# Optimization experiments

Hardware: AMD Instinct MI355X
Metric: run time of the kernel (lower is better)

The kernel has to match this reference:

```python
import jax, jax.numpy as jnp
import numpy as np

B, C, D = 16384, 2048, 128
POS_PROB = 0.002  # ~33 positives per class on average
EPS_POOL = 1e-9
EPS_NORM = 1e-12


def _l2_normalize(x, axis=-1):
    return x * jax.lax.rsqrt(jnp.sum(x * x, axis=axis, keepdims=True) + EPS_NORM)


def setup_inputs() -> dict:
    key = jax.random.key(0)
    k1, k2, k3 = jax.random.split(key, 3)
    output = jax.random.normal(k1, (B, D), dtype=jnp.float32)
    class_emb = jax.random.normal(k2, (C, D), dtype=jnp.float32)
    targets = (jax.random.uniform(k3, (B, C)) < POS_PROB).astype(jnp.float32)
    temperature = jnp.float32(0.07)
    return {"output": output, "class_emb": class_emb, "targets": targets,
            "temperature": temperature}


def reference(output, class_emb, targets, temperature):
    dt = output.dtype
    # masked mean pooling per class: equivalent to tile->mask->sum/count_nonzero
    # counts[c,d] = #{b : targets[b,c]*output[b,d] != 0}
    t_nz = (targets != 0).astype(dt)            # [B,C]
    o_nz = (output != 0).astype(dt)             # [B,D]
    counts = jnp.einsum('bc,bd->cd', t_nz, o_nz)          # [C,D]
    pooled = jnp.einsum('bc,bd->cd', targets, output) / (counts + EPS_POOL)  # [C,D]
    # cosine similarities (avoid materializing [C,C,D] tiles)
    pn = _l2_normalize(pooled)                  # [C,D]
    en = _l2_normalize(class_emb)               # [C,D]
    all_cosine = pn @ en.T                      # [C,C]
    class_sim = en @ en.T                       # [C,C]
    # topk(-sim, C) then argsort == rank of each class by ascending similarity
    order = jnp.argsort(class_sim, axis=-1)     # ascending sim (== topk of -sim)
    rank = jnp.argsort(order, axis=-1)          # inverse permutation
    discount = jnp.log(rank.astype(dt) + 2.0)   # [C,C]
    logits = all_cosine / (temperature * discount)
    log_p = jax.nn.log_softmax(logits, axis=1)  # [C,C]
    pos_log_p = jnp.diagonal(log_p)             # [C] diagonal gather
    mask_count = jnp.sum(targets, axis=0)       # [C]
    valid = mask_count > 0
    n_valid = jnp.maximum(jnp.sum(valid.astype(dt)), 1.0)
    infonce_mean = jnp.sum(jnp.where(valid, -pos_log_p, 0.0)) / n_valid
    return infonce_mean
```

## Files before the change

### kernel.cpp

```cpp
#include <hip/hip_runtime.h>
#include <hip/hip_bf16.h>
#include <math.h>

#define B_SZ 16384
#define C_SZ 2048
#define D_SZ 128
#define MAXP 256
#define SCAN_BLOCKS 4096

typedef float f32x4 __attribute__((ext_vector_type(4)));
typedef short short8 __attribute__((ext_vector_type(8)));


__global__ __launch_bounds__(256) void k_pre(unsigned* __restrict__ zr) {
    int t = blockIdx.x * blockDim.x + threadIdx.x;
    if (t < 2112) zr[t] = 0u;
}

__global__ __launch_bounds__(256) void k_scan(const float* __restrict__ targets,
                                              const float* __restrict__ class_emb,
                                              int* __restrict__ pos_count,
                                              int* __restrict__ pos_list,
                                              __hip_bfloat16* __restrict__ enh,
                                              __hip_bfloat16* __restrict__ enl) {
    const int bid = blockIdx.x;
    if (bid >= SCAN_BLOCKS) {
        const int g = threadIdx.x >> 7;
        const int d = threadIdx.x & 127;
        const int c = ((bid - SCAN_BLOCKS) << 1) + g;
        __shared__ float s_w[2][2];
        float v = class_emb[c * D_SZ + d];
        float sq = v * v;
#pragma unroll
        for (int off = 32; off >= 1; off >>= 1) sq += __shfl_xor(sq, off);
        if ((d & 63) == 0) s_w[g][d >> 6] = sq;
        __syncthreads();
        float tot = s_w[g][0] + s_w[g][1];
        float vn = v * rsqrtf(tot + 1e-12f);
        __hip_bfloat16 h = __float2bfloat16(vn);
        enh[c * D_SZ + d] = h;
        enl[c * D_SZ + d] = __float2bfloat16(vn - __bfloat162float(h));
        return;
    }
    int tid = bid * 256 + threadIdx.x;
    int total = (B_SZ * C_SZ) >> 2;
    const int stride = SCAN_BLOCKS * 256;
    for (int v = tid; v < total; v += stride) {
        float4 t = ((const float4*)targets)[v];
        if (t.x != 0.f || t.y != 0.f || t.z != 0.f || t.w != 0.f) {
            int e0 = v << 2;
            int b = e0 >> 11;
            int c0 = e0 & (C_SZ - 1);
            float vals[4] = {t.x, t.y, t.z, t.w};
#pragma unroll
            for (int q = 0; q < 4; ++q) {
                if (vals[q] != 0.f) {
                    int c = c0 + q;
                    int slot = atomicAdd(&pos_count[c], 1);
                    if (slot < MAXP) pos_list[c * MAXP + slot] = b;
                }
            }
        }
    }
}

__global__ __launch_bounds__(256) void k_pool(const float* __restrict__ output,
                                              const int* __restrict__ pos_count,
                                              const int* __restrict__ pos_list,
                                              __hip_bfloat16* __restrict__ pnh,
                                              __hip_bfloat16* __restrict__ pnl) {
    int c = blockIdx.x;
    int d = threadIdx.x & 127;
    int half = threadIdx.x >> 7;
    __shared__ float s_acc[2][128];
    __shared__ float s_cnt[2][128];
    __shared__ float s_w[2];
    int n = pos_count[c];
    if (n > MAXP) n = MAXP;
    float acc = 0.f, cnt = 0.f;
    for (int k = half; k < n; k += 2) {
        int b = pos_list[c * MAXP + k];
        float v = output[b * D_SZ + d];
        acc += v;
        cnt += (v != 0.f) ? 1.f : 0.f;
    }
    s_acc[half][d] = acc;
    s_cnt[half][d] = cnt;
    __syncthreads();
    if (half == 0) {
        acc = s_acc[0][d] + s_acc[1][d];
        cnt = s_cnt[0][d] + s_cnt[1][d];
        float pooled = acc / (cnt + 1e-9f);
        float sq = pooled * pooled;
#pragma unroll
        for (int off = 32; off >= 1; off >>= 1) sq += __shfl_xor(sq, off);
        if ((d & 63) == 0) s_w[d >> 6] = sq;
        __syncthreads();
        float tot = s_w[0] + s_w[1];
        float vn = pooled * rsqrtf(tot + 1e-12f);
        __hip_bfloat16 h = __float2bfloat16(vn);
        pnh[c * D_SZ + d] = h;
        pnl[c * D_SZ + d] = __float2bfloat16(vn - __bfloat162float(h));
    } else {
        __syncthreads();
    }
}

__global__ __launch_bounds__(256) void k_gemm_mfma(const __hip_bfloat16* __restrict__ enh_p,
                                                   const __hip_bfloat16* __restrict__ enl_p,
                                                   const __hip_bfloat16* __restrict__ pnh_p,
                                                   const __hip_bfloat16* __restrict__ pnl_p,
                                                   float* __restrict__ sim,
                                                   float* __restrict__ cosm) {
    extern __shared__ char smem[];
    char* As = smem;
    char* Bs = smem + 32768;
    const int tid = threadIdx.x;
    const __hip_bfloat16* Ah;
    const __hip_bfloat16* Al;
    float* Out;
    int rb;
    if (blockIdx.y < 32) { Ah = enh_p; Al = enl_p; Out = sim;  rb = blockIdx.y << 6; }
    else                 { Ah = pnh_p; Al = pnl_p; Out = cosm; rb = (blockIdx.y - 32) << 6; }
    const int cb = blockIdx.x << 6;
    {
        int r = tid >> 2;
        int c0 = (tid & 3) << 5;
        int sw = (r & 7) << 4;
#pragma unroll
        for (int j = 0; j < 4; ++j) {
            int c = c0 + (j << 3);
            uint4 vh = *(const uint4*)&Ah[(rb + r) * D_SZ + c];
            *(uint4*)(As + r * 512 + ((2 * c) ^ sw)) = vh;
            uint4 vl = *(const uint4*)&Al[(rb + r) * D_SZ + c];
            *(uint4*)(As + r * 512 + ((512 + 2 * c) ^ sw) - 256) = vl;
            uint4 wh = *(const uint4*)&enh_p[(cb + r) * D_SZ + c];
            *(uint4*)(Bs + r * 512 + ((2 * c) ^ sw)) = wh;
            uint4 wl = *(const uint4*)&enl_p[(cb + r) * D_SZ + c];
            *(uint4*)(Bs + r * 512 + ((512 + 2 * c) ^ sw) - 256) = wl;
        }
    }
    __syncthreads();
    const int w = tid >> 6, lane = tid & 63;
    const int wr = (w >> 1) << 5;
    const int wc = (w & 1) << 5;
    const int lrow = lane & 15;
    const int lk = (lane >> 4) << 4;
    int ar0 = wr + lrow, ar1 = wr + 16 + lrow;
    int br0 = wc + lrow, br1 = wc + 16 + lrow;
    const char* pa0 = As + ar0 * 512; const int swa0 = (ar0 & 7) << 4;
    const char* pa1 = As + ar1 * 512; const int swa1 = (ar1 & 7) << 4;
    const char* pb0 = Bs + br0 * 512; const int swb0 = (br0 & 7) << 4;
    const char* pb1 = Bs + br1 * 512; const int swb1 = (br1 & 7) << 4;
    f32x4 acc00 = {0.f, 0.f, 0.f, 0.f};
    f32x4 acc01 = acc00, acc10 = acc00, acc11 = acc00;
#pragma unroll
    for (int term = 0; term < 3; ++term) {
        const int ao = (term == 2) ? 256 : 0;
        const int bo = (term == 1) ? 256 : 0;
#pragma unroll
        for (int kk = 0; kk < 4; ++kk) {
            const int ka = ao + (kk << 6) + lk;
            const int kb = bo + (kk << 6) + lk;
            short8 a0 = *(const short8*)(pa0 + ((ka & 0x100) | ((ka & 0xFF) ^ swa0)));
            short8 a1 = *(const short8*)(pa1 + ((ka & 0x100) | ((ka & 0xFF) ^ swa1)));
            short8 b0 = *(const short8*)(pb0 + ((kb & 0x100) | ((kb & 0xFF) ^ swb0)));
            short8 b1 = *(const short8*)(pb1 + ((kb & 0x100) | ((kb & 0xFF) ^ swb1)));
            acc00 = __builtin_amdgcn_mfma_f32_16x16x32_bf16(a0, b0, acc00, 0, 0, 0);
            acc01 = __builtin_amdgcn_mfma_f32_16x16x32_bf16(a0, b1, acc01, 0, 0, 0);
            acc10 = __builtin_amdgcn_mfma_f32_16x16x32_bf16(a1, b0, acc10, 0, 0, 0);
            acc11 = __builtin_amdgcn_mfma_f32_16x16x32_bf16(a1, b1, acc11, 0, 0, 0);
        }
    }
    const int crow = rb + wr + ((lane >> 4) << 2);
    const int ccol = cb + wc + lrow;
#pragma unroll
    for (int r = 0; r < 4; ++r) {
        Out[(crow + r) * C_SZ + ccol]           = acc00[r];
        Out[(crow + r) * C_SZ + ccol + 16]      = acc01[r];
        Out[(crow + 16 + r) * C_SZ + ccol]      = acc10[r];
        Out[(crow + 16 + r) * C_SZ + ccol + 16] = acc11[r];
    }
}

__global__ __launch_bounds__(512) void k_rank_softmax(const float* __restrict__ sim,
                                                      const float* __restrict__ cosm,
                                                      const int* __restrict__ pos_count,
                                                      const float* __restrict__ tempPtr,
                                                      float* __restrict__ acc) {
    const int i0 = blockIdx.x << 1;
    __shared__ unsigned s_keys[2][C_SZ];
    __shared__ unsigned short s_idx[2][C_SZ];
    __shared__ unsigned s_hist[2][C_SZ / 2];
    __shared__ int s_wt[2][8];
    __shared__ float s_reds[2][8];
    __shared__ float s_diag[2];
    const int tid = threadIdx.x;
    const int lane = tid & 63;
    const int w = tid >> 6;
    const int base = tid << 2;
    const float M = 21.0f;
    const float temp = tempPtr[0];

    const bool v0 = pos_count[i0] != 0;
    const bool v1 = pos_count[i0 + 1] != 0;

    float4 sa0 = *(const float4*)&sim[i0 * C_SZ + base];
    float4 sa1 = *(const float4*)&sim[(i0 + 1) * C_SZ + base];
    float4 ca0 = *(const float4*)&cosm[i0 * C_SZ + base];
    float4 ca1 = *(const float4*)&cosm[(i0 + 1) * C_SZ + base];
    {
        uint4 z4 = {0u, 0u, 0u, 0u};
        ((uint4*)s_hist)[tid] = z4;
    }
    float xs0[4] = {sa0.x, sa0.y, sa0.z, sa0.w};
    float xs1[4] = {sa1.x, sa1.y, sa1.z, sa1.w};
    unsigned uk0[4], uk1[4];
    int bk0[4], bk1[4];
#pragma unroll
    for (int e = 0; e < 4; ++e) {
        unsigned u = __float_as_uint(xs0[e]);
        u = (u & 0x80000000u) ? ~u : (u | 0x80000000u);
        if (u == 0x7FFFFFFFu) u = 0x80000000u;
        uk0[e] = u;
        int b = (int)((xs0[e] + 0.5f) * 2047.0f);
        bk0[e] = b < 0 ? 0 : (b > 2047 ? 2047 : b);
        unsigned u1 = __float_as_uint(xs1[e]);
        u1 = (u1 & 0x80000000u) ? ~u1 : (u1 | 0x80000000u);
        if (u1 == 0x7FFFFFFFu) u1 = 0x80000000u;
        uk1[e] = u1;
        int b1 = (int)((xs1[e] + 0.5f) * 2047.0f);
        bk1[e] = b1 < 0 ? 0 : (b1 > 2047 ? 2047 : b1);
    }
    __syncthreads();
    if (v0) {
#pragma unroll
        for (int e = 0; e < 4; ++e)
            atomicAdd(&s_hist[0][bk0[e] >> 1], 1u << ((bk0[e] & 1) << 4));
    }
    if (v1) {
#pragma unroll
        for (int e = 0; e < 4; ++e)
            atomicAdd(&s_hist[1][bk1[e] >> 1], 1u << ((bk1[e] & 1) << 4));
    }
    __syncthreads();
    unsigned w00 = s_hist[0][2 * tid], w01 = s_hist[0][2 * tid + 1];
    unsigned w10 = s_hist[1][2 * tid], w11 = s_hist[1][2 * tid + 1];
    unsigned c00 = w00 & 0xFFFF, c01 = w00 >> 16, c02 = w01 & 0xFFFF, c03 = w01 >> 16;
    unsigned c10 = w10 & 0xFFFF, c11 = w10 >> 16, c12 = w11 & 0xFFFF, c13 = w11 >> 16;
    unsigned sum0 = c00 + c01 + c02 + c03;
    unsigned sum1 = c10 + c11 + c12 + c13;
    int incl0 = (int)sum0, incl1 = (int)sum1;
#pragma unroll
    for (int off = 1; off < 64; off <<= 1) {
        int o0 = __shfl_up(incl0, off);
        int o1 = __shfl_up(incl1, off);
        if (lane >= off) { incl0 += o0; incl1 += o1; }
    }
    if (lane == 63) { s_wt[0][w] = incl0; s_wt[1][w] = incl1; }
    __syncthreads();
    int wb0 = 0, wb1 = 0;
#pragma unroll
    for (int ww = 0; ww < 8; ++ww) {
        wb0 += (ww < w) ? s_wt[0][ww] : 0;
        wb1 += (ww < w) ? s_wt[1][ww] : 0;
    }
    unsigned eb0 = (unsigned)(wb0 + incl0 - (int)sum0);
    unsigned eb1 = (unsigned)(wb1 + incl1 - (int)sum1);
    {
        unsigned e00 = eb0, e01 = eb0 + c00, e02 = eb0 + c00 + c01, e03 = eb0 + c00 + c01 + c02;
        s_hist[0][2 * tid]     = e00 | (e01 << 16);
        s_hist[0][2 * tid + 1] = e02 | (e03 << 16);
        unsigned e10 = eb1, e11 = eb1 + c10, e12 = eb1 + c10 + c11, e13 = eb1 + c10 + c11 + c12;
        s_hist[1][2 * tid]     = e10 | (e11 << 16);
        s_hist[1][2 * tid + 1] = e12 | (e13 << 16);
    }
    __syncthreads();
    if (v0) {
#pragma unroll
        for (int e = 0; e < 4; ++e) {
            int sh = (bk0[e] & 1) << 4;
            unsigned old = atomicAdd(&s_hist[0][bk0[e] >> 1], 1u << sh);
            unsigned pos = (old >> sh) & 0xFFFFu;
            s_keys[0][pos] = uk0[e];
            s_idx[0][pos] = (unsigned short)(base + e);
        }
    }
    if (v1) {
#pragma unroll
        for (int e = 0; e < 4; ++e) {
            int sh = (bk1[e] & 1) << 4;
            unsigned old = atomicAdd(&s_hist[1][bk1[e] >> 1], 1u << sh);
            unsigned pos = (old >> sh) & 0xFFFFu;
            s_keys[1][pos] = uk1[e];
            s_idx[1][pos] = (unsigned short)(base + e);
        }
    }
    __syncthreads();
    float ls0 = 0.f, ls1 = 0.f;
    float cs0[4] = {ca0.x, ca0.y, ca0.z, ca0.w};
    float cs1[4] = {ca1.x, ca1.y, ca1.z, ca1.w};
    if (v0) {
        float lg0[4];
#pragma unroll
        for (int e = 0; e < 4; ++e) {
            int b = bk0[e];
            unsigned endv = (s_hist[0][b >> 1] >> ((b & 1) << 4)) & 0xFFFFu;
            unsigned startv = b ? ((s_hist[0][(b - 1) >> 1] >> (((b - 1) & 1) << 4)) & 0xFFFFu) : 0u;
            unsigned mk = uk0[e];
            int less = 0, eq = 0;
            for (unsigned j = startv; j < endv; ++j) {
                unsigned kj = s_keys[0][j];
                less += (kj < mk) ? 1 : 0;
                eq += (kj == mk) ? 1 : 0;
            }
            if (eq > 1) {
                unsigned myi = (unsigned)(base + e);
                for (unsigned j = startv; j < endv; ++j)
                    if (s_keys[0][j] == mk && (unsigned)s_idx[0][j] < myi) less++;
            }
            int rk = (int)startv + less;
            float den = temp * __logf((float)rk + 2.0f);
            lg0[e] = __fdividef(cs0[e], den);
            ls0 += __expf(lg0[e] - M);
        }
        if ((i0 >> 2) == tid) {
            int ei = i0 & 3;
            float dv = lg0[0];
#pragma unroll
            for (int e = 1; e < 4; ++e) dv = (ei == e) ? lg0[e] : dv;
            s_diag[0] = dv;
        }
    }
    if (v1) {
        float lg1[4];
#pragma unroll
        for (int e = 0; e < 4; ++e) {
            int b = bk1[e];
            unsigned endv = (s_hist[1][b >> 1] >> ((b & 1) << 4)) & 0xFFFFu;
            unsigned startv = b ? ((s_hist[1][(b - 1) >> 1] >> (((b - 1) & 1) << 4)) & 0xFFFFu) : 0u;
            unsigned mk = uk1[e];
            int less = 0, eq = 0;
            for (unsigned j = startv; j < endv; ++j) {
                unsigned kj = s_keys[1][j];
                less += (kj < mk) ? 1 : 0;
                eq += (kj == mk) ? 1 : 0;
            }
            if (eq > 1) {
                unsigned myi = (unsigned)(base + e);
                for (unsigned j = startv; j < endv; ++j)
                    if (s_keys[1][j] == mk && (unsigned)s_idx[1][j] < myi) less++;
            }
            int rk = (int)startv + less;
            float den = temp * __logf((float)rk + 2.0f);
            lg1[e] = __fdividef(cs1[e], den);
            ls1 += __expf(lg1[e] - M);
        }
        if (((i0 + 1) >> 2) == tid) {
            int ei = (i0 + 1) & 3;
            float dv = lg1[0];
#pragma unroll
            for (int e = 1; e < 4; ++e) dv = (ei == e) ? lg1[e] : dv;
            s_diag[1] = dv;
        }
    }
#pragma unroll
    for (int off = 1; off < 64; off <<= 1) {
        ls0 += __shfl_xor(ls0, off);
        ls1 += __shfl_xor(ls1, off);
    }
    if (lane == 0) { s_reds[0][w] = ls0; s_reds[1][w] = ls1; }
    __syncthreads();
    if (tid == 0) {
        float t0 = 0.f, t1 = 0.f;
#pragma unroll
        for (int ww = 0; ww < 8; ++ww) { t0 += s_reds[0][ww]; t1 += s_reds[1][ww]; }
        float lp = 0.f, nv = 0.f;
        if (v0) { lp += -(s_diag[0] - M - logf(t0)); nv += 1.f; }
        if (v1) { lp += -(s_diag[1] - M - logf(t1)); nv += 1.f; }
        if (nv > 0.f) {
            atomicAdd(&acc[0], lp);
            atomicAdd(&acc[1], nv);
        }
    }
}

__global__ void k_final(const float* __restrict__ acc, float* __restrict__ out) {
    out[0] = acc[0] / fmaxf(acc[1], 1.0f);
}

extern "C" void kernel_launch(void* const* d_in, const int* in_sizes, int n_in,
                              void* d_out, int out_size, void* d_ws, size_t ws_size,
                              hipStream_t stream) {
    const float* output    = (const float*)d_in[0];
    const float* class_emb = (const float*)d_in[1];
    const float* targets   = (const float*)d_in[2];
    const float* tempPtr   = (const float*)d_in[3];
    float* out = (float*)d_out;
    char* ws = (char*)d_ws;

    int*   pos_count = (int*)(ws + 0);
    float* acc       = (float*)(ws + 8192);
    int*   pos_list  = (int*)(ws + 8448);
    __hip_bfloat16* pnh = (__hip_bfloat16*)(ws + 2105600);
    __hip_bfloat16* pnl = (__hip_bfloat16*)(ws + 2629888);
    __hip_bfloat16* enh = (__hip_bfloat16*)(ws + 3154176);
    __hip_bfloat16* enl = (__hip_bfloat16*)(ws + 3678464);
    float* sim       = (float*)(ws + 4210944);
    float* cosm      = (float*)(ws + 20988160);

    k_pre<<<9, 256, 0, stream>>>((unsigned*)ws);
    k_scan<<<SCAN_BLOCKS + C_SZ / 2, 256, 0, stream>>>(targets, class_emb,
                                                       pos_count, pos_list, enh, enl);
    k_pool<<<C_SZ, 256, 0, stream>>>(output, pos_count, pos_list, pnh, pnl);
    dim3 g(C_SZ / 64, 2 * C_SZ / 64);
    k_gemm_mfma<<<g, 256, 65536, stream>>>(enh, enl, pnh, pnl, sim, cosm);
    k_rank_softmax<<<C_SZ / 2, 512, 0, stream>>>(sim, cosm, pos_count, tempPtr, acc);
    k_final<<<1, 1, 0, stream>>>(acc, out);
}
```

Baseline: 105.0 us.

## Rewrite rank-softmax as one-wavefront-per-row kernel with per-row partials and block reduction

```diff
diff --git a/kernel.cpp b/kernel.cpp
--- a/kernel.cpp
+++ b/kernel.cpp
@@ -14,7 +14,7 @@
 
 __global__ __launch_bounds__(256) void k_pre(unsigned* __restrict__ zr) {
     int t = blockIdx.x * blockDim.x + threadIdx.x;
-    if (t < 2112) zr[t] = 0u;
+    if (t < C_SZ) zr[t] = 0u;
 }
 
 __global__ __launch_bounds__(256) void k_scan(const float* __restrict__ targets,
@@ -183,210 +183,158 @@
     }
 }
 
-__global__ __launch_bounds__(512) void k_rank_softmax(const float* __restrict__ sim,
-                                                      const float* __restrict__ cosm,
-                                                      const int* __restrict__ pos_count,
-                                                      const float* __restrict__ tempPtr,
-                                                      float* __restrict__ acc) {
-    const int i0 = blockIdx.x << 1;
-    __shared__ unsigned s_keys[2][C_SZ];
-    __shared__ unsigned short s_idx[2][C_SZ];
-    __shared__ unsigned s_hist[2][C_SZ / 2];
-    __shared__ int s_wt[2][8];
-    __shared__ float s_reds[2][8];
-    __shared__ float s_diag[2];
-    const int tid = threadIdx.x;
-    const int lane = tid & 63;
-    const int w = tid >> 6;
-    const int base = tid << 2;
+__device__ __forceinline__ int bucket_of(unsigned u) {
+    float x = (u & 0x80000000u) ? __uint_as_float(u & 0x7FFFFFFFu)
+                                : __uint_as_float(~u);
+    int b = (int)((x + 0.5f) * 2047.0f);
+    return b < 0 ? 0 : (b > 2047 ? 2047 : b);
+}
+
+__global__ __launch_bounds__(64) void k_rank_softmax(const float* __restrict__ sim,
+                                                     const float* __restrict__ cosm,
+                                                     const int* __restrict__ pos_count,
+                                                     const float* __restrict__ tempPtr,
+                                                     float* __restrict__ partial) {
+    const int i = blockIdx.x;
+    const int lane = threadIdx.x;
+    if (pos_count[i] == 0) {
+        if (lane == 0) { partial[2 * i] = 0.f; partial[2 * i + 1] = 0.f; }
+        return;
+    }
+    __shared__ unsigned s_keys[C_SZ];
+    __shared__ unsigned s_hist[C_SZ / 2];
     const float M = 21.0f;
     const float temp = tempPtr[0];
-
-    const bool v0 = pos_count[i0] != 0;
-    const bool v1 = pos_count[i0 + 1] != 0;
-
-    float4 sa0 = *(const float4*)&sim[i0 * C_SZ + base];
-    float4 sa1 = *(const float4*)&sim[(i0 + 1) * C_SZ + base];
-    float4 ca0 = *(const float4*)&cosm[i0 * C_SZ + base];
-    float4 ca1 = *(const float4*)&cosm[(i0 + 1) * C_SZ + base];
     {
-        uint4 z4 = {0u, 0u, 0u, 0u};
-        ((uint4*)s_hist)[tid] = z4;
-    }
-    float xs0[4] = {sa0.x, sa0.y, sa0.z, sa0.w};
-    float xs1[4] = {sa1.x, sa1.y, sa1.z, sa1.w};
-    unsigned uk0[4], uk1[4];
-    int bk0[4], bk1[4];
-#pragma unroll
-    for (int e = 0; e < 4; ++e) {
-        unsigned u = __float_as_uint(xs0[e]);
-        u = (u & 0x80000000u) ? ~u : (u | 0x80000000u);
-        if (u == 0x7FFFFFFFu) u = 0x80000000u;
-        uk0[e] = u;
-        int b = (int)((xs0[e] + 0.5f) * 2047.0f);
-        bk0[e] = b < 0 ? 0 : (b > 2047 ? 2047 : b);
-        unsigned u1 = __float_as_uint(xs1[e]);
-        u1 = (u1 & 0x80000000u) ? ~u1 : (u1 | 0x80000000u);
-        if (u1 == 0x7FFFFFFFu) u1 = 0x80000000u;
-        uk1[e] = u1;
-        int b1 = (int)((xs1[e] + 0.5f) * 2047.0f);
-        bk1[e] = b1 < 0 ? 0 : (b1 > 2047 ? 2047 : b1);
-    }
-    __syncthreads();
-    if (v0) {
-#pragma unroll
-        for (int e = 0; e < 4; ++e)
-            atomicAdd(&s_hist[0][bk0[e] >> 1], 1u << ((bk0[e] & 1) << 4));
-    }
-    if (v1) {
-#pragma unroll
-        for (int e = 0; e < 4; ++e)
-            atomicAdd(&s_hist[1][bk1[e] >> 1], 1u << ((bk1[e] & 1) << 4));
-    }
-    __syncthreads();
-    unsigned w00 = s_hist[0][2 * tid], w01 = s_hist[0][2 * tid + 1];
-    unsigned w10 = s_hist[1][2 * tid], w11 = s_hist[1][2 * tid + 1];
-    unsigned c00 = w00 & 0xFFFF, c01 = w00 >> 16, c02 = w01 & 0xFFFF, c03 = w01 >> 16;
-    unsigned c10 = w10 & 0xFFFF, c11 = w10 >> 16, c12 = w11 & 0xFFFF, c13 = w11 >> 16;
-    unsigned sum0 = c00 + c01 + c02 + c03;
-    unsigned sum1 = c10 + c11 + c12 + c13;
-    int incl0 = (int)sum0, incl1 = (int)sum1;
+        uint4 z = {0u, 0u, 0u, 0u};
+#pragma unroll
+        for (int k = 0; k < 4; ++k) ((uint4*)s_hist)[k * 64 + lane] = z;
+    }
+    __syncthreads();
+    unsigned uk[32];
+#pragma unroll
+    for (int k = 0; k < 8; ++k) {
+        float4 v = *(const float4*)&sim[i * C_SZ + k * 256 + lane * 4];
+        float xs[4] = {v.x, v.y, v.z, v.w};
+#pragma unroll
+        for (int q = 0; q < 4; ++q) {
+            unsigned u = __float_as_uint(xs[q]);
+            u = (u & 0x80000000u) ? ~u : (u | 0x80000000u);
+            if (u == 0x7FFFFFFFu) u = 0x80000000u;
+            uk[k * 4 + q] = u;
+            int b = (int)((xs[q] + 0.5f) * 2047.0f);
+            b = b < 0 ? 0 : (b > 2047 ? 2047 : b);
+            atomicAdd(&s_hist[b >> 1], 1u << ((b & 1) << 4));
+        }
+    }
+    __syncthreads();
+    unsigned w[16];
+#pragma unroll
+    for (int k = 0; k < 4; ++k) {
+        uint4 t = ((const uint4*)s_hist)[lane * 4 + k];
+        w[k * 4 + 0] = t.x; w[k * 4 + 1] = t.y; w[k * 4 + 2] = t.z; w[k * 4 + 3] = t.w;
+    }
+    unsigned tot = 0;
+#pragma unroll
+    for (int k = 0; k < 16; ++k) tot += (w[k] & 0xFFFFu) + (w[k] >> 16);
+    int incl = (int)tot;
 #pragma unroll
     for (int off = 1; off < 64; off <<= 1) {
-        int o0 = __shfl_up(incl0, off);
-        int o1 = __shfl_up(incl1, off);
-        if (lane >= off) { incl0 += o0; incl1 += o1; }
-    }
-    if (lane == 63) { s_wt[0][w] = incl0; s_wt[1][w] = incl1; }
-    __syncthreads();
-    int wb0 = 0, wb1 = 0;
-#pragma unroll
-    for (int ww = 0; ww < 8; ++ww) {
-        wb0 += (ww < w) ? s_wt[0][ww] : 0;
-        wb1 += (ww < w) ? s_wt[1][ww] : 0;
-    }
-    unsigned eb0 = (unsigned)(wb0 + incl0 - (int)sum0);
-    unsigned eb1 = (unsigned)(wb1 + incl1 - (int)sum1);
-    {
-        unsigned e00 = eb0, e01 = eb0 + c00, e02 = eb0 + c00 + c01, e03 = eb0 + c00 + c01 + c02;
-        s_hist[0][2 * tid]     = e00 | (e01 << 16);
-        s_hist[0][2 * tid + 1] = e02 | (e03 << 16);
-        unsigned e10 = eb1, e11 = eb1 + c10, e12 = eb1 + c10 + c11, e13 = eb1 + c10 + c11 + c12;
-        s_hist[1][2 * tid]     = e10 | (e11 << 16);
-        s_hist[1][2 * tid + 1] = e12 | (e13 << 16);
-    }
-    __syncthreads();
-    if (v0) {
-#pragma unroll
-        for (int e = 0; e < 4; ++e) {
-            int sh = (bk0[e] & 1) << 4;
-            unsigned old = atomicAdd(&s_hist[0][bk0[e] >> 1], 1u << sh);
-            unsigned pos = (old >> sh) & 0xFFFFu;
-            s_keys[0][pos] = uk0[e];
-            s_idx[0][pos] = (unsigned short)(base + e);
-        }
-    }
-    if (v1) {
-#pragma unroll
-        for (int e = 0; e < 4; ++e) {
-            int sh = (bk1[e] & 1) << 4;
-            unsigned old = atomicAdd(&s_hist[1][bk1[e] >> 1], 1u << sh);
-            unsigned pos = (old >> sh) & 0xFFFFu;
-            s_keys[1][pos] = uk1[e];
-            s_idx[1][pos] = (unsigned short)(base + e);
-        }
-    }
-    __syncthreads();
-    float ls0 = 0.f, ls1 = 0.f;
-    float cs0[4] = {ca0.x, ca0.y, ca0.z, ca0.w};
-    float cs1[4] = {ca1.x, ca1.y, ca1.z, ca1.w};
-    if (v0) {
-        float lg0[4];
-#pragma unroll
-        for (int e = 0; e < 4; ++e) {
-            int b = bk0[e];
-            unsigned endv = (s_hist[0][b >> 1] >> ((b & 1) << 4)) & 0xFFFFu;
-            unsigned startv = b ? ((s_hist[0][(b - 1) >> 1] >> (((b - 1) & 1) << 4)) & 0xFFFFu) : 0u;
-            unsigned mk = uk0[e];
-            int less = 0, eq = 0;
-            for (unsigned j = startv; j < endv; ++j) {
-                unsigned kj = s_keys[0][j];
-                less += (kj < mk) ? 1 : 0;
-                eq += (kj == mk) ? 1 : 0;
+        int o = __shfl_up(incl, off);
+        if (lane >= off) incl += o;
+    }
+    unsigned run = (unsigned)incl - tot;
+#pragma unroll
+    for (int k = 0; k < 16; ++k) {
+        unsigned lo = w[k] & 0xFFFFu, hi = w[k] >> 16;
+        unsigned e_lo = run; run += lo;
+        unsigned e_hi = run; run += hi;
+        s_hist[lane * 16 + k] = e_lo | (e_hi << 16);
+    }
+    __syncthreads();
+    float cs[32];
+#pragma unroll
+    for (int k = 0; k < 8; ++k) {
+        float4 v = *(const float4*)&cosm[i * C_SZ + k * 256 + lane * 4];
+        cs[k * 4 + 0] = v.x; cs[k * 4 + 1] = v.y; cs[k * 4 + 2] = v.z; cs[k * 4 + 3] = v.w;
+    }
+#pragma unroll
+    for (int e = 0; e < 32; ++e) {
+        int b = bucket_of(uk[e]);
+        int sh = (b & 1) << 4;
+        unsigned old = atomicAdd(&s_hist[b >> 1], 1u << sh);
+        unsigned pos = (old >> sh) & 0xFFFFu;
+        s_keys[pos] = uk[e];
+    }
+    __syncthreads();
+    float ls = 0.f;
+    float diag = -3.4e38f;
+#pragma unroll
+    for (int e = 0; e < 32; ++e) {
+        unsigned mk = uk[e];
+        int b = bucket_of(mk);
+        unsigned hw = s_hist[b >> 1];
+        unsigned endv = (hw >> ((b & 1) << 4)) & 0xFFFFu;
+        unsigned startv = 0;
+        if (b > 0) {
+            unsigned pw = (b & 1) ? hw : s_hist[(b - 1) >> 1];
+            startv = (pw >> (((b - 1) & 1) << 4)) & 0xFFFFu;
+        }
+        int less = 0, eq = 0;
+        for (unsigned j = startv; j < endv; ++j) {
+            unsigned kj = s_keys[j];
+            less += (kj < mk) ? 1 : 0;
+            eq += (kj == mk) ? 1 : 0;
+        }
+        int myidx = ((e >> 2) << 8) + (lane << 2) + (e & 3);
+        if (eq > 1) {
+            for (int j = 0; j < myidx; ++j) {
+                unsigned u = __float_as_uint(sim[i * C_SZ + j]);
+                u = (u & 0x80000000u) ? ~u : (u | 0x80000000u);
+                if (u == 0x7FFFFFFFu) u = 0x80000000u;
+                less += (u == mk) ? 1 : 0;
             }
-            if (eq > 1) {
-                unsigned myi = (unsigned)(base + e);
-                for (unsigned j = startv; j < endv; ++j)
-                    if (s_keys[0][j] == mk && (unsigned)s_idx[0][j] < myi) less++;
-            }
-            int rk = (int)startv + less;
-            float den = temp * __logf((float)rk + 2.0f);
-            lg0[e] = __fdividef(cs0[e], den);
-            ls0 += __expf(lg0[e] - M);
-        }
-        if ((i0 >> 2) == tid) {
-            int ei = i0 & 3;
-            float dv = lg0[0];
-#pragma unroll
-            for (int e = 1; e < 4; ++e) dv = (ei == e) ? lg0[e] : dv;
-            s_diag[0] = dv;
-        }
-    }
-    if (v1) {
-        float lg1[4];
-#pragma unroll
-        for (int e = 0; e < 4; ++e) {
-            int b = bk1[e];
-            unsigned endv = (s_hist[1][b >> 1] >> ((b & 1) << 4)) & 0xFFFFu;
-            unsigned startv = b ? ((s_hist[1][(b - 1) >> 1] >> (((b - 1) & 1) << 4)) & 0xFFFFu) : 0u;
-            unsigned mk = uk1[e];
-            int less = 0, eq = 0;
-            for (unsigned j = startv; j < endv; ++j) {
-                unsigned kj = s_keys[1][j];
-                less += (kj < mk) ? 1 : 0;
-                eq += (kj == mk) ? 1 : 0;
-            }
-            if (eq > 1) {
-                unsigned myi = (unsigned)(base + e);
-                for (unsigned j = startv; j < endv; ++j)
-                    if (s_keys[1][j] == mk && (unsigned)s_idx[1][j] < myi) less++;
-            }
-            int rk = (int)startv + less;
-            float den = temp * __logf((float)rk + 2.0f);
-            lg1[e] = __fdividef(cs1[e], den);
-            ls1 += __expf(lg1[e] - M);
-        }
-        if (((i0 + 1) >> 2) == tid) {
-            int ei = (i0 + 1) & 3;
-            float dv = lg1[0];
-#pragma unroll
-            for (int e = 1; e < 4; ++e) dv = (ei == e) ? lg1[e] : dv;
-            s_diag[1] = dv;
-        }
+        }
+        int rk = (int)startv + less;
+        float lg = __fdividef(cs[e], temp * __logf((float)rk + 2.0f));
+        ls += __expf(lg - M);
+        if (myidx == i) diag = lg;
     }
 #pragma unroll
     for (int off = 1; off < 64; off <<= 1) {
-        ls0 += __shfl_xor(ls0, off);
-        ls1 += __shfl_xor(ls1, off);
-    }
-    if (lane == 0) { s_reds[0][w] = ls0; s_reds[1][w] = ls1; }
-    __syncthreads();
-    if (tid == 0) {
-        float t0 = 0.f, t1 = 0.f;
-#pragma unroll
-        for (int ww = 0; ww < 8; ++ww) { t0 += s_reds[0][ww]; t1 += s_reds[1][ww]; }
-        float lp = 0.f, nv = 0.f;
-        if (v0) { lp += -(s_diag[0] - M - logf(t0)); nv += 1.f; }
-        if (v1) { lp += -(s_diag[1] - M - logf(t1)); nv += 1.f; }
-        if (nv > 0.f) {
-            atomicAdd(&acc[0], lp);
-            atomicAdd(&acc[1], nv);
-        }
-    }
-}
-
-__global__ void k_final(const float* __restrict__ acc, float* __restrict__ out) {
-    out[0] = acc[0] / fmaxf(acc[1], 1.0f);
+        ls += __shfl_xor(ls, off);
+        diag = fmaxf(diag, __shfl_xor(diag, off));
+    }
+    if (lane == 0) {
+        partial[2 * i]     = -(diag - M - logf(ls));
+        partial[2 * i + 1] = 1.f;
+    }
+}
+
+__global__ __launch_bounds__(256) void k_final(const float* __restrict__ partial,
+                                               float* __restrict__ out) {
+    const int t = threadIdx.x;
+    const int lane = t & 63;
+    const int w = t >> 6;
+    __shared__ float s_lp[4], s_nv[4];
+    float lp = 0.f, nv = 0.f;
+#pragma unroll
+    for (int k = 0; k < 8; ++k) {
+        float2 p = ((const float2*)partial)[k * 256 + t];
+        lp += p.x; nv += p.y;
+    }
+#pragma unroll
+    for (int off = 1; off < 64; off <<= 1) {
+        lp += __shfl_xor(lp, off);
+        nv += __shfl_xor(nv, off);
+    }
+    if (lane == 0) { s_lp[w] = lp; s_nv[w] = nv; }
+    __syncthreads();
+    if (t == 0) {
+        float slp = s_lp[0] + s_lp[1] + s_lp[2] + s_lp[3];
+        float snv = s_nv[0] + s_nv[1] + s_nv[2] + s_nv[3];
+        out[0] = slp / fmaxf(snv, 1.0f);
+    }
 }
 
 extern "C" void kernel_launch(void* const* d_in, const int* in_sizes, int n_in,
@@ -400,7 +348,6 @@
     char* ws = (char*)d_ws;
 
     int*   pos_count = (int*)(ws + 0);
-    float* acc       = (float*)(ws + 8192);
     int*   pos_list  = (int*)(ws + 8448);
     __hip_bfloat16* pnh = (__hip_bfloat16*)(ws + 2105600);
     __hip_bfloat16* pnl = (__hip_bfloat16*)(ws + 2629888);
@@ -408,13 +355,14 @@
     __hip_bfloat16* enl = (__hip_bfloat16*)(ws + 3678464);
     float* sim       = (float*)(ws + 4210944);
     float* cosm      = (float*)(ws + 20988160);
-
-    k_pre<<<9, 256, 0, stream>>>((unsigned*)ws);
+    float* partial   = (float*)(ws + 37765376);
+
+    k_pre<<<8, 256, 0, stream>>>((unsigned*)ws);
     k_scan<<<SCAN_BLOCKS + C_SZ / 2, 256, 0, stream>>>(targets, class_emb,
                                                        pos_count, pos_list, enh, enl);
     k_pool<<<C_SZ, 256, 0, stream>>>(output, pos_count, pos_list, pnh, pnl);
     dim3 g(C_SZ / 64, 2 * C_SZ / 64);
     k_gemm_mfma<<<g, 256, 65536, stream>>>(enh, enl, pnh, pnl, sim, cosm);
-    k_rank_softmax<<<C_SZ / 2, 512, 0, stream>>>(sim, cosm, pos_count, tempPtr, acc);
-    k_final<<<1, 1, 0, stream>>>(acc, out);
-}
+    k_rank_softmax<<<C_SZ, 64, 0, stream>>>(sim, cosm, pos_count, tempPtr, partial);
+    k_final<<<1, 256, 0, stream>>>(partial, out);
+}
```

New measurement: 353.7 us. +236.8%, slower.
